# Performance work log

Measured on AMD Instinct MI355X. Metric: run time of the kernel, lower is better.

## Reference

```python
import jax, jax.numpy as jnp
import numpy as np

NUM_EXPERTS = 8
HIDDEN = 1024
INTER = 1024
BATCH = 2
SEQ = 1024
TOP_K = 2
SWIGLU_ALPHA = 1.702
LIMIT = 7.0


def setup_inputs() -> dict:
    key = jax.random.key(0)
    ks = jax.random.split(key, 7)
    hidden_states = jax.random.normal(ks[0], (BATCH, SEQ, HIDDEN), jnp.float32)
    router_indices = jax.random.randint(ks[1], (BATCH * SEQ, TOP_K), 0, NUM_EXPERTS)
    routing_weights = jax.nn.softmax(
        jax.random.normal(ks[2], (BATCH * SEQ, NUM_EXPERTS), jnp.float32), axis=-1)
    scale = 0.02
    gate_up_proj = jax.random.normal(ks[3], (NUM_EXPERTS, HIDDEN, 2 * INTER), jnp.float32) * scale
    gate_up_proj_bias = jax.random.normal(ks[4], (NUM_EXPERTS, 2 * INTER), jnp.float32) * scale
    down_proj = jax.random.normal(ks[5], (NUM_EXPERTS, INTER, HIDDEN), jnp.float32) * scale
    down_proj_bias = jax.random.normal(ks[6], (NUM_EXPERTS, HIDDEN), jnp.float32) * scale
    return {
        "hidden_states": hidden_states,
        "router_indices": router_indices,
        "routing_weights": routing_weights,
        "gate_up_proj": gate_up_proj,
        "gate_up_proj_bias": gate_up_proj_bias,
        "down_proj": down_proj,
        "down_proj_bias": down_proj_bias,
    }


def _grouped_mm(x, w, expert_ids):
    """Grouped GEMM: y[t] = x[t] @ w[expert_ids[t]].

    x: [T, K], w: [E, K, N], expert_ids: [T] int.
    Reference form via one-hot masking (exact equivalent of torch._grouped_mm
    on expert-sorted tokens); guaranteed jit- and grad-safe.
    """
    onehot = jax.nn.one_hot(expert_ids, w.shape[0], dtype=x.dtype)  # [T, E]
    y_all = jnp.einsum('tk,ekn->etn', x, w)                         # [E, T, N]
    return jnp.einsum('te,etn->tn', onehot, y_all)                  # [T, N]


def _gpt_oss_swiglu(x):
    gate = jnp.minimum(x[..., ::2], LIMIT)
    up = jnp.clip(x[..., 1::2], -LIMIT, LIMIT)
    glu = gate * jax.nn.sigmoid(gate * SWIGLU_ALPHA)
    return (up + 1.0) * glu


def reference(hidden_states, router_indices, routing_weights,
              gate_up_proj, gate_up_proj_bias, down_proj, down_proj_bias):
    B = hidden_states.shape[0]
    H = hidden_states.shape[-1]
    x = hidden_states.reshape(-1, H)                       # [M, H]
    M = x.shape[0]
    top_k = router_indices.shape[1]
    num_experts = gate_up_proj.shape[0]

    # routing_weights is [M, num_experts] -> gather the top-k weights
    topk_weights = jnp.take_along_axis(routing_weights, router_indices, axis=1)  # [M, K]

    flat_experts = router_indices.reshape(-1)              # [T = M*K]
    sort_idx = jnp.argsort(flat_experts)                   # expert-sorted order
    sorted_pos = sort_idx // top_k                         # token id per slot
    expert_sorted = flat_experts[sort_idx]                 # [T]
    grouped = x[sorted_pos]                                # [T, H]

    gate_up = _grouped_mm(grouped, gate_up_proj, expert_sorted)
    gate_up = gate_up + gate_up_proj_bias[expert_sorted]   # per-expert bias
    inter = _gpt_oss_swiglu(gate_up)                       # [T, I]

    down = _grouped_mm(inter, down_proj, expert_sorted)
    down = down + down_proj_bias[expert_sorted]            # [T, H]
    down = down * topk_weights.reshape(-1)[sort_idx][:, None]

    out = jnp.zeros((M, H), x.dtype).at[sorted_pos].add(down)  # scatter-add combine
    return out.reshape(B, -1, H)
```

## Files before the change

### kernel.cpp

```cpp
#include <hip/hip_runtime.h>

#define NE 8
#define NH 1024
#define NI 1024
#define NGU 2048
#define MTOK 2048
#define TSLOT 4096

#define MAXT64 80
#define MAXT128 40

typedef short s16x8 __attribute__((ext_vector_type(8)));
typedef float f32x4 __attribute__((ext_vector_type(4)));
typedef unsigned short u16;

#define WS_SEG      0
#define WS_DESC64   64
#define WS_DESC128  384
#define WS_SLOT     1024
#define WS_POS      17408
#define WS_INTER    33792
#define WS_AREG     8422400UL
#define WS_WREG     25199616UL
#define WS_NEED_FAST 58754048UL

__device__ inline u16 f2bf(float f) {
    unsigned u = __builtin_bit_cast(unsigned, f);
    u += 0x7fffu + ((u >> 16) & 1u);
    return (u16)(u >> 16);
}

__device__ inline void lds_dma16(const u16* g, u16* l) {
    __builtin_amdgcn_global_load_lds(
        (const __attribute__((address_space(1))) unsigned int*)g,
        (__attribute__((address_space(3))) unsigned int*)l, 16, 0, 0);
}

__device__ inline int lds_off(int row, int blk) {
    return (row << 7) | (((blk ^ (row & 7)) & 7) << 4);
}

__global__ void k_build(const int* __restrict__ ridx, int* __restrict__ seg,
                        int* __restrict__ d64, int* __restrict__ d128,
                        int* __restrict__ slot_of, int* __restrict__ pos_of) {
    __shared__ int cnt[NE];
    __shared__ int cur[NE];
    int tid = threadIdx.x;
    if (tid < NE) cnt[tid] = 0;
    __syncthreads();
    for (int s = tid; s < TSLOT; s += blockDim.x) atomicAdd(&cnt[ridx[s] & 7], 1);
    __syncthreads();
    if (tid == 0) {
        int a = 0;
        for (int e = 0; e < NE; ++e) { seg[e] = a; cur[e] = a; a += cnt[e]; }
        seg[NE] = a;
        int nt = 0;
        for (int e = 0; e < NE; ++e)
            for (int m0 = 0; m0 < cnt[e]; m0 += 64) d64[nt++] = (e << 16) | (m0 / 64);
        for (; nt < MAXT64; ++nt) d64[nt] = -1;
        nt = 0;
        for (int e = 0; e < NE; ++e)
            for (int m0 = 0; m0 < cnt[e]; m0 += 128) d128[nt++] = (e << 16) | (m0 / 128);
        for (; nt < MAXT128; ++nt) d128[nt] = -1;
    }
    __syncthreads();
    for (int s = tid; s < TSLOT; s += blockDim.x) {
        int e = ridx[s] & 7;
        int p = atomicAdd(&cur[e], 1);
        slot_of[p] = s;
        pos_of[s] = p;
    }
}

__global__ __launch_bounds__(256) void k_gather(const float* __restrict__ x,
                                                const int* __restrict__ slot_of,
                                                u16* __restrict__ A) {
    int r = blockIdx.x;
    int token = slot_of[r] >> 1;
    float4 v = ((const float4*)(x + (size_t)token * NH))[threadIdx.x];
    ushort4 o;
    o.x = f2bf(v.x); o.y = f2bf(v.y); o.z = f2bf(v.z); o.w = f2bf(v.w);
    ((ushort4*)(A + (size_t)r * NH))[threadIdx.x] = o;
}

__global__ __launch_bounds__(256) void k_tr(const float* __restrict__ W,
                                            u16* __restrict__ WT, int K, int N) {
    __shared__ u16 T[64][66];
    int tid = threadIdx.x;
    const float* in = W + (size_t)blockIdx.z * K * N;
    u16* out = WT + (size_t)blockIdx.z * N * K;
    int n0 = blockIdx.x * 64, k0 = blockIdx.y * 64;
#pragma unroll
    for (int p = 0; p < 2; ++p) {
        int kr = p * 32 + (tid >> 4) * 2;
        int nc = (tid & 15) * 4;
        const float* r0 = in + (size_t)(k0 + kr) * N + n0 + nc;
        float4 v0 = *(const float4*)r0;
        float4 v1 = *(const float4*)(r0 + N);
#pragma unroll
        for (int i = 0; i < 4; ++i) {
            unsigned lo = f2bf(((const float*)&v0)[i]);
            unsigned hi = f2bf(((const float*)&v1)[i]);
            *(unsigned*)&T[nc + i][kr] = lo | (hi << 16);
        }
    }
    __syncthreads();
#pragma unroll
    for (int p = 0; p < 2; ++p) {
        int idx = p * 256 + tid;
        int nr = idx >> 3, kc = (idx & 7) * 8;
        unsigned q0 = *(const unsigned*)&T[nr][kc + 0];
        unsigned q1 = *(const unsigned*)&T[nr][kc + 2];
        unsigned q2 = *(const unsigned*)&T[nr][kc + 4];
        unsigned q3 = *(const unsigned*)&T[nr][kc + 6];
        uint4 vv = {q0, q1, q2, q3};
        *(uint4*)(out + (size_t)(n0 + nr) * K + k0 + kc) = vv;
    }
}

__global__ __launch_bounds__(256) void k_gateup_f(
        const u16* __restrict__ A,
        const u16* __restrict__ wt,
        const float* __restrict__ bias,
        const int* __restrict__ seg, const int* __restrict__ desc,
        u16* __restrict__ inter) {
    int d = desc[blockIdx.x];
    if (d < 0) return;
    int e = d >> 16, mt = d & 0xffff;
    int seg0 = seg[e], Te = seg[e + 1] - seg0, m0 = mt * 128;

    __shared__ __align__(16) u16 As[128 * 64];
    __shared__ __align__(16) u16 Bs[128 * 64];

    int tid = threadIdx.x;
    int lane = tid & 63, w = tid >> 6;
    int ml = lane & 15, kq = lane >> 4;
    int wm = w >> 1, wn = w & 1;
    int n0 = blockIdx.y * 128;
    const u16* wte = wt + (size_t)e * NGU * NH;
    int dr = lane >> 3, db = (lane & 7) ^ dr;

    f32x4 zero = {0.f, 0.f, 0.f, 0.f};
    f32x4 acc[4][4];
#pragma unroll
    for (int i = 0; i < 4; ++i)
#pragma unroll
        for (int j = 0; j < 4; ++j) acc[i][j] = zero;

    for (int kb = 0; kb < NH; kb += 64) {
        __syncthreads();
#pragma unroll
        for (int c = 0; c < 4; ++c) {
            int gr = seg0 + m0 + c * 32 + w * 8 + dr;
            if (gr > TSLOT - 1) gr = TSLOT - 1;
            lds_dma16(A + (size_t)gr * NH + kb + db * 8, As + c * 2048 + w * 512);
        }
#pragma unroll
        for (int c = 0; c < 4; ++c) {
            int row = c * 32 + w * 8 + dr;
            lds_dma16(wte + (size_t)(n0 + row) * NH + kb + db * 8, Bs + c * 2048 + w * 512);
        }
        __syncthreads();

#pragma unroll
        for (int kk = 0; kk < 64; kk += 32) {
            s16x8 af[4], bf[4];
#pragma unroll
            for (int i = 0; i < 4; ++i)
                af[i] = *(const s16x8*)((char*)As + lds_off(wm * 64 + i * 16 + ml, (kk >> 3) + kq));
#pragma unroll
            for (int i = 0; i < 4; ++i)
                bf[i] = *(const s16x8*)((char*)Bs + lds_off(wn * 64 + i * 16 + ml, (kk >> 3) + kq));
#pragma unroll
            for (int mi = 0; mi < 4; ++mi)
#pragma unroll
                for (int ni = 0; ni < 4; ++ni)
                    acc[mi][ni] = __builtin_amdgcn_mfma_f32_16x16x32_bf16(
                        af[mi], bf[ni], acc[mi][ni], 0, 0, 0);
        }
    }

#pragma unroll
    for (int ni = 0; ni < 4; ++ni) {
        int n = n0 + wn * 64 + ni * 16 + ml;
        float bv = bias[e * NGU + n];
#pragma unroll
        for (int mi = 0; mi < 4; ++mi) {
#pragma unroll
            for (int r = 0; r < 4; ++r) {
                float v = acc[mi][ni][r] + bv;
                float pr = __shfl_xor(v, 1, 64);
                float g = (lane & 1) ? pr : v;
                float u = (lane & 1) ? v : pr;
                g = fminf(g, 7.0f);
                u = fminf(fmaxf(u, -7.0f), 7.0f);
                float glu = g / (1.0f + __expf(-1.702f * g));
                float y = (u + 1.0f) * glu;
                int mloc = wm * 64 + mi * 16 + kq * 4 + r;
                if (!(lane & 1) && (m0 + mloc) < Te)
                    inter[(size_t)(seg0 + m0 + mloc) * NI + (n >> 1)] = f2bf(y);
            }
        }
    }
}

__global__ __launch_bounds__(256) void k_down_f(
        const u16* __restrict__ inter,
        const u16* __restrict__ wt,
        const float* __restrict__ bias,
        const float* __restrict__ rw,
        const int* __restrict__ seg, const int* __restrict__ desc,
        const int* __restrict__ slot_of,
        float* __restrict__ out) {
    int d = desc[blockIdx.x];
    if (d < 0) return;
    int e = d >> 16, mt = d & 0xffff;
    int seg0 = seg[e], Te = seg[e + 1] - seg0, m0 = mt * 128;

    __shared__ __align__(16) u16 As[128 * 64];
    __shared__ __align__(16) u16 Bs[128 * 64];
    __shared__ int tokS[128];
    __shared__ float wgtS[128];

    int tid = threadIdx.x;
    if (tid < 128) {
        int m = m0 + tid;
        if (m < Te) {
            int token = slot_of[seg0 + m] >> 1;
            tokS[tid] = token;
            wgtS[tid] = rw[token * NE + e];
        } else {
            tokS[tid] = 0;
            wgtS[tid] = 0.0f;
        }
    }

    int lane = tid & 63, w = tid >> 6;
    int ml = lane & 15, kq = lane >> 4;
    int wm = w >> 1, wn = w & 1;
    int n0 = blockIdx.y * 128;
    const u16* wte = wt + (size_t)e * NH * NI;
    int dr = lane >> 3, db = (lane & 7) ^ dr;

    f32x4 zero = {0.f, 0.f, 0.f, 0.f};
    f32x4 acc[4][4];
#pragma unroll
    for (int i = 0; i < 4; ++i)
#pragma unroll
        for (int j = 0; j < 4; ++j) acc[i][j] = zero;

    for (int kb = 0; kb < NI; kb += 64) {
        __syncthreads();
#pragma unroll
        for (int c = 0; c < 4; ++c) {
            int gr = seg0 + m0 + c * 32 + w * 8 + dr;
            if (gr > TSLOT - 1) gr = TSLOT - 1;
            lds_dma16(inter + (size_t)gr * NI + kb + db * 8, As + c * 2048 + w * 512);
        }
#pragma unroll
        for (int c = 0; c < 4; ++c) {
            int row = c * 32 + w * 8 + dr;
            lds_dma16(wte + (size_t)(n0 + row) * NI + kb + db * 8, Bs + c * 2048 + w * 512);
        }
        __syncthreads();

#pragma unroll
        for (int kk = 0; kk < 64; kk += 32) {
            s16x8 af[4], bf[4];
#pragma unroll
            for (int i = 0; i < 4; ++i)
                af[i] = *(const s16x8*)((char*)As + lds_off(wm * 64 + i * 16 + ml, (kk >> 3) + kq));
#pragma unroll
            for (int i = 0; i < 4; ++i)
                bf[i] = *(const s16x8*)((char*)Bs + lds_off(wn * 64 + i * 16 + ml, (kk >> 3) + kq));
#pragma unroll
            for (int mi = 0; mi < 4; ++mi)
#pragma unroll
                for (int ni = 0; ni < 4; ++ni)
                    acc[mi][ni] = __builtin_amdgcn_mfma_f32_16x16x32_bf16(
                        af[mi], bf[ni], acc[mi][ni], 0, 0, 0);
        }
    }

    float bv[4];
#pragma unroll
    for (int ni = 0; ni < 4; ++ni)
        bv[ni] = bias[e * NH + n0 + wn * 64 + ni * 16 + ml];

#pragma unroll
    for (int mi = 0; mi < 4; ++mi) {
#pragma unroll
        for (int r = 0; r < 4; ++r) {
            int mloc = wm * 64 + mi * 16 + kq * 4 + r;
            if ((m0 + mloc) < Te) {
                int token = tokS[mloc];
                float wgt = wgtS[mloc];
#pragma unroll
                for (int ni = 0; ni < 4; ++ni) {
                    int n = n0 + wn * 64 + ni * 16 + ml;
                    atomicAdd(&out[(size_t)token * NH + n], (acc[mi][ni][r] + bv[ni]) * wgt);
                }
            }
        }
    }
}

__global__ __launch_bounds__(256) void k_gateup_s(
        const float* __restrict__ x, const float* __restrict__ w,
        const float* __restrict__ bias,
        const int* __restrict__ seg, const int* __restrict__ desc,
        const int* __restrict__ slot_of, u16* __restrict__ inter) {
    int d = desc[blockIdx.x];
    if (d < 0) return;
    int e = d >> 16, mt = d & 0xffff;
    int seg0 = seg[e], Te = seg[e + 1] - seg0, m0 = mt * 64;
    __shared__ u16 As[64 * 40];
    __shared__ int tok[64];
    int tid = threadIdx.x;
    if (tid < 64) {
        int m = m0 + tid;
        tok[tid] = (m < Te) ? (slot_of[seg0 + m] >> 1) : -1;
    }
    __syncthreads();
    int lane = tid & 63, wave = tid >> 6;
    int arow = tid >> 2, acol = (tid & 3) * 8;
    int ta = tok[arow];
    int kq = lane >> 4, ml = lane & 15;
    int nb = blockIdx.y * 128 + wave * 32;
    const float* wp = w + (size_t)e * NH * NGU;
    f32x4 zero = {0.f, 0.f, 0.f, 0.f};
    f32x4 acc[4][2];
#pragma unroll
    for (int i = 0; i < 4; ++i) { acc[i][0] = zero; acc[i][1] = zero; }
    for (int kb = 0; kb < NH; kb += 32) {
        float4 a0 = {0, 0, 0, 0}, a1 = {0, 0, 0, 0};
        if (ta >= 0) {
            const float* xp = x + (size_t)ta * NH + kb + acol;
            a0 = *(const float4*)xp; a1 = *(const float4*)(xp + 4);
        }
        s16x8 av;
        av[0] = (short)f2bf(a0.x); av[1] = (short)f2bf(a0.y);
        av[2] = (short)f2bf(a0.z); av[3] = (short)f2bf(a0.w);
        av[4] = (short)f2bf(a1.x); av[5] = (short)f2bf(a1.y);
        av[6] = (short)f2bf(a1.z); av[7] = (short)f2bf(a1.w);
        __syncthreads();
        *(s16x8*)&As[arow * 40 + acol] = av;
        __syncthreads();
        s16x8 afr[4];
#pragma unroll
        for (int msi = 0; msi < 4; ++msi)
            afr[msi] = *(const s16x8*)&As[(msi * 16 + ml) * 40 + kq * 8];
        s16x8 bfr[2];
#pragma unroll
        for (int s = 0; s < 2; ++s) {
            const float* bp = wp + (size_t)(kb + kq * 8) * NGU + nb + s * 16 + ml;
#pragma unroll
            for (int j = 0; j < 8; ++j) bfr[s][j] = (short)f2bf(bp[(size_t)j * NGU]);
        }
#pragma unroll
        for (int msi = 0; msi < 4; ++msi)
#pragma unroll
            for (int s = 0; s < 2; ++s)
                acc[msi][s] = __builtin_amdgcn_mfma_f32_16x16x32_bf16(
                    afr[msi], bfr[s], acc[msi][s], 0, 0, 0);
    }
#pragma unroll
    for (int s = 0; s < 2; ++s) {
        int n = nb + s * 16 + ml;
        float bv = bias[e * NGU + n];
#pragma unroll
        for (int msi = 0; msi < 4; ++msi) {
#pragma unroll
            for (int r = 0; r < 4; ++r) {
                float v = acc[msi][s][r] + bv;
                float pr = __shfl_xor(v, 1, 64);
                float g = (lane & 1) ? pr : v;
                float u = (lane & 1) ? v : pr;
                g = fminf(g, 7.0f);
                u = fminf(fmaxf(u, -7.0f), 7.0f);
                float glu = g / (1.0f + __expf(-1.702f * g));
                float y = (u + 1.0f) * glu;
                int mrow = m0 + msi * 16 + kq * 4 + r;
                if (!(lane & 1) && mrow < Te)
                    inter[(size_t)(seg0 + mrow) * NI + (n >> 1)] = f2bf(y);
            }
        }
    }
}

__global__ __launch_bounds__(256) void k_down_s(
        const u16* __restrict__ inter, const float* __restrict__ w,
        const float* __restrict__ bias, const float* __restrict__ rw,
        const int* __restrict__ seg, const int* __restrict__ desc,
        const int* __restrict__ slot_of, float* __restrict__ out) {
    int d = desc[blockIdx.x];
    if (d < 0) return;
    int e = d >> 16, mt = d & 0xffff;
    int seg0 = seg[e], Te = seg[e + 1] - seg0, m0 = mt * 64;
    __shared__ u16 As[64 * 40];
    int tid = threadIdx.x;
    int lane = tid & 63, wave = tid >> 6;
    int arow = tid >> 2, acol = (tid & 3) * 8;
    bool avalid = (m0 + arow) < Te;
    int kq = lane >> 4, ml = lane & 15;
    int nb = blockIdx.y * 128 + wave * 32;
    const float* wp = w + (size_t)e * NI * NH;
    f32x4 zero = {0.f, 0.f, 0.f, 0.f};
    f32x4 acc[4][2];
#pragma unroll
    for (int i = 0; i < 4; ++i) { acc[i][0] = zero; acc[i][1] = zero; }
    for (int kb = 0; kb < NI; kb += 32) {
        s16x8 av = {0, 0, 0, 0, 0, 0, 0, 0};
        if (avalid) av = *(const s16x8*)(inter + (size_t)(seg0 + m0 + arow) * NI + kb + acol);
        __syncthreads();
        *(s16x8*)&As[arow * 40 + acol] = av;
        __syncthreads();
        s16x8 afr[4];
#pragma unroll
        for (int msi = 0; msi < 4; ++msi)
            afr[msi] = *(const s16x8*)&As[(msi * 16 + ml) * 40 + kq * 8];
        s16x8 bfr[2];
#pragma unroll
        for (int s = 0; s < 2; ++s) {
            const float* bp = wp + (size_t)(kb + kq * 8) * NH + nb + s * 16 + ml;
#pragma unroll
            for (int j = 0; j < 8; ++j) bfr[s][j] = (short)f2bf(bp[(size_t)j * NH]);
        }
#pragma unroll
        for (int msi = 0; msi < 4; ++msi)
#pragma unroll
            for (int s = 0; s < 2; ++s)
                acc[msi][s] = __builtin_amdgcn_mfma_f32_16x16x32_bf16(
                    afr[msi], bfr[s], acc[msi][s], 0, 0, 0);
    }
    float bv[2];
    bv[0] = bias[e * NH + nb + ml];
    bv[1] = bias[e * NH + nb + 16 + ml];
#pragma unroll
    for (int msi = 0; msi < 4; ++msi) {
#pragma unroll
        for (int r = 0; r < 4; ++r) {
            int mrow = m0 + msi * 16 + kq * 4 + r;
            if (mrow < Te) {
                int slot = slot_of[seg0 + mrow];
                int token = slot >> 1;
                float wgt = rw[token * NE + e];
#pragma unroll
                for (int s = 0; s < 2; ++s) {
                    int n = nb + s * 16 + ml;
                    atomicAdd(&out[(size_t)token * NH + n], (acc[msi][s][r] + bv[s]) * wgt);
                }
            }
        }
    }
}

extern "C" void kernel_launch(void* const* d_in, const int* in_sizes, int n_in,
                              void* d_out, int out_size, void* d_ws, size_t ws_size,
                              hipStream_t stream) {
    const float* x   = (const float*)d_in[0];
    const int*   ri  = (const int*)d_in[1];
    const float* rw  = (const float*)d_in[2];
    const float* wgu = (const float*)d_in[3];
    const float* bgu = (const float*)d_in[4];
    const float* wd  = (const float*)d_in[5];
    const float* bd  = (const float*)d_in[6];
    float* out = (float*)d_out;

    char* ws = (char*)d_ws;
    int* seg     = (int*)(ws + WS_SEG);
    int* d64     = (int*)(ws + WS_DESC64);
    int* d128    = (int*)(ws + WS_DESC128);
    int* slot_of = (int*)(ws + WS_SLOT);
    int* pos_of  = (int*)(ws + WS_POS);
    u16* inter   = (u16*)(ws + WS_INTER);

    hipLaunchKernelGGL(k_build, dim3(1), dim3(256), 0, stream, ri, seg, d64, d128,
                       slot_of, pos_of);
    hipMemsetAsync(out, 0, (size_t)MTOK * NH * sizeof(float), stream);

    if (ws_size >= WS_NEED_FAST) {
        u16* aReg = (u16*)(ws + WS_AREG);
        u16* wReg = (u16*)(ws + WS_WREG);
        hipLaunchKernelGGL(k_tr, dim3(NGU / 64, NH / 64, NE), dim3(256), 0, stream,
                           wgu, wReg, NH, NGU);
        hipLaunchKernelGGL(k_gather, dim3(TSLOT), dim3(256), 0, stream, x, slot_of, aReg);
        hipLaunchKernelGGL(k_gateup_f, dim3(MAXT128, NGU / 128), dim3(256), 0, stream,
                           aReg, wReg, bgu, seg, d128, inter);
        hipLaunchKernelGGL(k_tr, dim3(NH / 64, NI / 64, NE), dim3(256), 0, stream,
                           wd, wReg, NI, NH);
        hipLaunchKernelGGL(k_down_f, dim3(MAXT128, NH / 128), dim3(256), 0, stream,
                           inter, wReg, bd, rw, seg, d128, slot_of, out);
    } else {
        hipLaunchKernelGGL(k_gateup_s, dim3(MAXT64, NGU / 128), dim3(256), 0, stream,
                           x, wgu, bgu, seg, d64, slot_of, inter);
        hipLaunchKernelGGL(k_down_s, dim3(MAXT64, NH / 128), dim3(256), 0, stream,
                           inter, wd, bd, rw, seg, d64, slot_of, out);
    }
}
```

Measured before the change: 251.8 us.

## Double-buffer LDS in grouped GEMMs, halve N tile, split-K the down projection

Both fast-path grouped GEMM kernels now prefetch the next K tile into a second LDS buffer via global_load_lds. The loop waits on partial vmcnt and uses raw barriers with setprio around the MFMA work, so loads overlap compute. The N tile is halved from 128 to 64 to launch more blocks, and the down kernel is split over K into two z-slices that both atomically add into the output, with bias added only by slice 0. This gives more parallelism and latency hiding, in exchange for lower per-block reuse of the A tile and twice the atomic traffic in the down projection.

```diff
diff --git a/kernel.cpp b/kernel.cpp
--- a/kernel.cpp
+++ b/kernel.cpp
@@ -39,6 +39,10 @@
 __device__ inline int lds_off(int row, int blk) {
     return (row << 7) | (((blk ^ (row & 7)) & 7) << 4);
 }
+
+#define PIPE_FENCE asm volatile("" ::: "memory")
+#define WAIT_VM6   asm volatile("s_waitcnt vmcnt(6)" ::: "memory")
+#define WAIT_VM0   asm volatile("s_waitcnt vmcnt(0)" ::: "memory")
 
 __global__ void k_build(const int* __restrict__ ridx, int* __restrict__ seg,
                         int* __restrict__ d64, int* __restrict__ d128,
@@ -129,60 +133,91 @@
     int e = d >> 16, mt = d & 0xffff;
     int seg0 = seg[e], Te = seg[e + 1] - seg0, m0 = mt * 128;
 
-    __shared__ __align__(16) u16 As[128 * 64];
-    __shared__ __align__(16) u16 Bs[128 * 64];
+    __shared__ __align__(16) u16 As0[128 * 64];
+    __shared__ __align__(16) u16 As1[128 * 64];
+    __shared__ __align__(16) u16 Bs0[64 * 64];
+    __shared__ __align__(16) u16 Bs1[64 * 64];
 
     int tid = threadIdx.x;
     int lane = tid & 63, w = tid >> 6;
     int ml = lane & 15, kq = lane >> 4;
     int wm = w >> 1, wn = w & 1;
-    int n0 = blockIdx.y * 128;
+    int n0 = blockIdx.y * 64;
     const u16* wte = wt + (size_t)e * NGU * NH;
     int dr = lane >> 3, db = (lane & 7) ^ dr;
 
+    const u16* aptr[4];
+#pragma unroll
+    for (int c = 0; c < 4; ++c) {
+        int gr = seg0 + m0 + c * 32 + w * 8 + dr;
+        if (gr > TSLOT - 1) gr = TSLOT - 1;
+        aptr[c] = A + (size_t)gr * NH + db * 8;
+    }
+    const u16* bptr[2];
+#pragma unroll
+    for (int c = 0; c < 2; ++c)
+        bptr[c] = wte + (size_t)(n0 + c * 32 + w * 8 + dr) * NH + db * 8;
+
+    auto stage = [&](u16* AS, u16* BS, int kb) {
+#pragma unroll
+        for (int c = 0; c < 4; ++c) lds_dma16(aptr[c] + kb, AS + c * 2048 + w * 512);
+#pragma unroll
+        for (int c = 0; c < 2; ++c) lds_dma16(bptr[c] + kb, BS + c * 2048 + w * 512);
+    };
+
     f32x4 zero = {0.f, 0.f, 0.f, 0.f};
-    f32x4 acc[4][4];
-#pragma unroll
-    for (int i = 0; i < 4; ++i)
-#pragma unroll
-        for (int j = 0; j < 4; ++j) acc[i][j] = zero;
-
-    for (int kb = 0; kb < NH; kb += 64) {
-        __syncthreads();
-#pragma unroll
-        for (int c = 0; c < 4; ++c) {
-            int gr = seg0 + m0 + c * 32 + w * 8 + dr;
-            if (gr > TSLOT - 1) gr = TSLOT - 1;
-            lds_dma16(A + (size_t)gr * NH + kb + db * 8, As + c * 2048 + w * 512);
-        }
-#pragma unroll
-        for (int c = 0; c < 4; ++c) {
-            int row = c * 32 + w * 8 + dr;
-            lds_dma16(wte + (size_t)(n0 + row) * NH + kb + db * 8, Bs + c * 2048 + w * 512);
-        }
-        __syncthreads();
-
+    f32x4 acc[4][2];
+#pragma unroll
+    for (int i = 0; i < 4; ++i) { acc[i][0] = zero; acc[i][1] = zero; }
+
+    auto compute = [&](const u16* AS, const u16* BS) {
 #pragma unroll
         for (int kk = 0; kk < 64; kk += 32) {
-            s16x8 af[4], bf[4];
+            s16x8 af[4], bf[2];
 #pragma unroll
             for (int i = 0; i < 4; ++i)
-                af[i] = *(const s16x8*)((char*)As + lds_off(wm * 64 + i * 16 + ml, (kk >> 3) + kq));
-#pragma unroll
-            for (int i = 0; i < 4; ++i)
-                bf[i] = *(const s16x8*)((char*)Bs + lds_off(wn * 64 + i * 16 + ml, (kk >> 3) + kq));
+                af[i] = *(const s16x8*)((const char*)AS + lds_off(wm * 64 + i * 16 + ml, (kk >> 3) + kq));
+#pragma unroll
+            for (int i = 0; i < 2; ++i)
+                bf[i] = *(const s16x8*)((const char*)BS + lds_off(wn * 32 + i * 16 + ml, (kk >> 3) + kq));
 #pragma unroll
             for (int mi = 0; mi < 4; ++mi)
 #pragma unroll
-                for (int ni = 0; ni < 4; ++ni)
+                for (int ni = 0; ni < 2; ++ni)
                     acc[mi][ni] = __builtin_amdgcn_mfma_f32_16x16x32_bf16(
                         af[mi], bf[ni], acc[mi][ni], 0, 0, 0);
         }
-    }
-
-#pragma unroll
-    for (int ni = 0; ni < 4; ++ni) {
-        int n = n0 + wn * 64 + ni * 16 + ml;
+    };
+
+    stage(As0, Bs0, 0);
+    for (int t = 0; t < 16; t += 2) {
+        stage(As1, Bs1, (t + 1) << 6);
+        WAIT_VM6;
+        __builtin_amdgcn_s_barrier();
+        PIPE_FENCE;
+        __builtin_amdgcn_s_setprio(1);
+        compute(As0, Bs0);
+        __builtin_amdgcn_s_setprio(0);
+        PIPE_FENCE;
+        __builtin_amdgcn_s_barrier();
+        if (t < 14) {
+            stage(As0, Bs0, (t + 2) << 6);
+            WAIT_VM6;
+        } else {
+            WAIT_VM0;
+        }
+        __builtin_amdgcn_s_barrier();
+        PIPE_FENCE;
+        __builtin_amdgcn_s_setprio(1);
+        compute(As1, Bs1);
+        __builtin_amdgcn_s_setprio(0);
+        PIPE_FENCE;
+        __builtin_amdgcn_s_barrier();
+    }
+
+#pragma unroll
+    for (int ni = 0; ni < 2; ++ni) {
+        int n = n0 + wn * 32 + ni * 16 + ml;
         float bv = bias[e * NGU + n];
 #pragma unroll
         for (int mi = 0; mi < 4; ++mi) {
@@ -216,9 +251,12 @@
     if (d < 0) return;
     int e = d >> 16, mt = d & 0xffff;
     int seg0 = seg[e], Te = seg[e + 1] - seg0, m0 = mt * 128;
-
-    __shared__ __align__(16) u16 As[128 * 64];
-    __shared__ __align__(16) u16 Bs[128 * 64];
+    int kz = blockIdx.z;
+
+    __shared__ __align__(16) u16 As0[128 * 64];
+    __shared__ __align__(16) u16 As1[128 * 64];
+    __shared__ __align__(16) u16 Bs0[64 * 64];
+    __shared__ __align__(16) u16 Bs1[64 * 64];
     __shared__ int tokS[128];
     __shared__ float wgtS[128];
 
@@ -238,54 +276,84 @@
     int lane = tid & 63, w = tid >> 6;
     int ml = lane & 15, kq = lane >> 4;
     int wm = w >> 1, wn = w & 1;
-    int n0 = blockIdx.y * 128;
+    int n0 = blockIdx.y * 64;
     const u16* wte = wt + (size_t)e * NH * NI;
     int dr = lane >> 3, db = (lane & 7) ^ dr;
+    int kbeg = kz * (NI / 2);
+
+    const u16* aptr[4];
+#pragma unroll
+    for (int c = 0; c < 4; ++c) {
+        int gr = seg0 + m0 + c * 32 + w * 8 + dr;
+        if (gr > TSLOT - 1) gr = TSLOT - 1;
+        aptr[c] = inter + (size_t)gr * NI + db * 8;
+    }
+    const u16* bptr[2];
+#pragma unroll
+    for (int c = 0; c < 2; ++c)
+        bptr[c] = wte + (size_t)(n0 + c * 32 + w * 8 + dr) * NI + db * 8;
+
+    auto stage = [&](u16* AS, u16* BS, int kb) {
+#pragma unroll
+        for (int c = 0; c < 4; ++c) lds_dma16(aptr[c] + kb, AS + c * 2048 + w * 512);
+#pragma unroll
+        for (int c = 0; c < 2; ++c) lds_dma16(bptr[c] + kb, BS + c * 2048 + w * 512);
+    };
 
     f32x4 zero = {0.f, 0.f, 0.f, 0.f};
-    f32x4 acc[4][4];
-#pragma unroll
-    for (int i = 0; i < 4; ++i)
-#pragma unroll
-        for (int j = 0; j < 4; ++j) acc[i][j] = zero;
-
-    for (int kb = 0; kb < NI; kb += 64) {
-        __syncthreads();
-#pragma unroll
-        for (int c = 0; c < 4; ++c) {
-            int gr = seg0 + m0 + c * 32 + w * 8 + dr;
-            if (gr > TSLOT - 1) gr = TSLOT - 1;
-            lds_dma16(inter + (size_t)gr * NI + kb + db * 8, As + c * 2048 + w * 512);
-        }
-#pragma unroll
-        for (int c = 0; c < 4; ++c) {
-            int row = c * 32 + w * 8 + dr;
-            lds_dma16(wte + (size_t)(n0 + row) * NI + kb + db * 8, Bs + c * 2048 + w * 512);
-        }
-        __syncthreads();
-
+    f32x4 acc[4][2];
+#pragma unroll
+    for (int i = 0; i < 4; ++i) { acc[i][0] = zero; acc[i][1] = zero; }
+
+    auto compute = [&](const u16* AS, const u16* BS) {
 #pragma unroll
         for (int kk = 0; kk < 64; kk += 32) {
-            s16x8 af[4], bf[4];
+            s16x8 af[4], bf[2];
 #pragma unroll
             for (int i = 0; i < 4; ++i)
-                af[i] = *(const s16x8*)((char*)As + lds_off(wm * 64 + i * 16 + ml, (kk >> 3) + kq));
-#pragma unroll
-            for (int i = 0; i < 4; ++i)
-                bf[i] = *(const s16x8*)((char*)Bs + lds_off(wn * 64 + i * 16 + ml, (kk >> 3) + kq));
+                af[i] = *(const s16x8*)((const char*)AS + lds_off(wm * 64 + i * 16 + ml, (kk >> 3) + kq));
+#pragma unroll
+            for (int i = 0; i < 2; ++i)
+                bf[i] = *(const s16x8*)((const char*)BS + lds_off(wn * 32 + i * 16 + ml, (kk >> 3) + kq));
 #pragma unroll
             for (int mi = 0; mi < 4; ++mi)
 #pragma unroll
-                for (int ni = 0; ni < 4; ++ni)
+                for (int ni = 0; ni < 2; ++ni)
                     acc[mi][ni] = __builtin_amdgcn_mfma_f32_16x16x32_bf16(
                         af[mi], bf[ni], acc[mi][ni], 0, 0, 0);
         }
-    }
-
-    float bv[4];
-#pragma unroll
-    for (int ni = 0; ni < 4; ++ni)
-        bv[ni] = bias[e * NH + n0 + wn * 64 + ni * 16 + ml];
+    };
+
+    stage(As0, Bs0, kbeg);
+    for (int t = 0; t < 8; t += 2) {
+        stage(As1, Bs1, kbeg + ((t + 1) << 6));
+        WAIT_VM6;
+        __builtin_amdgcn_s_barrier();
+        PIPE_FENCE;
+        __builtin_amdgcn_s_setprio(1);
+        compute(As0, Bs0);
+        __builtin_amdgcn_s_setprio(0);
+        PIPE_FENCE;
+        __builtin_amdgcn_s_barrier();
+        if (t < 6) {
+            stage(As0, Bs0, kbeg + ((t + 2) << 6));
+            WAIT_VM6;
+        } else {
+            WAIT_VM0;
+        }
+        __builtin_amdgcn_s_barrier();
+        PIPE_FENCE;
+        __builtin_amdgcn_s_setprio(1);
+        compute(As1, Bs1);
+        __builtin_amdgcn_s_setprio(0);
+        PIPE_FENCE;
+        __builtin_amdgcn_s_barrier();
+    }
+
+    float bv[2];
+#pragma unroll
+    for (int ni = 0; ni < 2; ++ni)
+        bv[ni] = kz ? 0.0f : bias[e * NH + n0 + wn * 32 + ni * 16 + ml];
 
 #pragma unroll
     for (int mi = 0; mi < 4; ++mi) {
@@ -296,8 +364,8 @@
                 int token = tokS[mloc];
                 float wgt = wgtS[mloc];
 #pragma unroll
-                for (int ni = 0; ni < 4; ++ni) {
-                    int n = n0 + wn * 64 + ni * 16 + ml;
+                for (int ni = 0; ni < 2; ++ni) {
+                    int n = n0 + wn * 32 + ni * 16 + ml;
                     atomicAdd(&out[(size_t)token * NH + n], (acc[mi][ni][r] + bv[ni]) * wgt);
                 }
             }
@@ -485,11 +553,11 @@
         hipLaunchKernelGGL(k_tr, dim3(NGU / 64, NH / 64, NE), dim3(256), 0, stream,
                            wgu, wReg, NH, NGU);
         hipLaunchKernelGGL(k_gather, dim3(TSLOT), dim3(256), 0, stream, x, slot_of, aReg);
-        hipLaunchKernelGGL(k_gateup_f, dim3(MAXT128, NGU / 128), dim3(256), 0, stream,
+        hipLaunchKernelGGL(k_gateup_f, dim3(MAXT128, NGU / 64), dim3(256), 0, stream,
                            aReg, wReg, bgu, seg, d128, inter);
         hipLaunchKernelGGL(k_tr, dim3(NH / 64, NI / 64, NE), dim3(256), 0, stream,
                            wd, wReg, NI, NH);
-        hipLaunchKernelGGL(k_down_f, dim3(MAXT128, NH / 128), dim3(256), 0, stream,
+        hipLaunchKernelGGL(k_down_f, dim3(MAXT128, NH / 64, 2), dim3(256), 0, stream,
                            inter, wReg, bd, rw, seg, d128, slot_of, out);
     } else {
         hipLaunchKernelGGL(k_gateup_s, dim3(MAXT64, NGU / 128), dim3(256), 0, stream,
```

Result: no change. 248.3 us (-1.4%).
